# Kernel tuning notes

Hardware: AMD Instinct MI355X
Metric: run time of the kernel (lower is better)

## Reference

```python
import jax, jax.numpy as jnp
import numpy as np

NUM_HEADS = 8
NUM_LEVELS = 4
NUM_POINTS = 16
NUM_BEV = 2
EMBED = 256
BS = 64
NQ = NUM_LEVELS * NUM_POINTS  # 64


def _bilinear_sample(img, grid):
    """F.grid_sample(mode='bilinear', padding_mode='zeros', align_corners=False).
    img: (N, C, H, W); grid: (N, Hg, Wg, 2) in [-1, 1] (x, y). Returns (N, C, Hg, Wg)."""
    N, C, H, W = img.shape
    gx = (grid[..., 0] + 1.0) * (W * 0.5) - 0.5  # (N, Hg, Wg)
    gy = (grid[..., 1] + 1.0) * (H * 0.5) - 0.5
    x0 = jnp.floor(gx)
    y0 = jnp.floor(gy)
    flat = img.reshape(N, C, H * W)

    def gather(xi, yi):
        valid = (xi >= 0) & (xi <= W - 1) & (yi >= 0) & (yi <= H - 1)
        xc = jnp.clip(xi, 0, W - 1).astype(jnp.int32)
        yc = jnp.clip(yi, 0, H - 1).astype(jnp.int32)
        idx = (yc * W + xc).reshape(N, 1, -1)
        g = jnp.take_along_axis(flat, idx, axis=2).reshape(N, C, xi.shape[1], xi.shape[2])
        return g * valid[:, None, :, :].astype(img.dtype)

    wx1 = (gx - x0)[:, None]  # (N,1,Hg,Wg)
    wy1 = (gy - y0)[:, None]
    v00 = gather(x0, y0)
    v01 = gather(x0 + 1.0, y0)
    v10 = gather(x0, y0 + 1.0)
    v11 = gather(x0 + 1.0, y0 + 1.0)
    top = v00 * (1.0 - wx1) + v01 * wx1
    bot = v10 * (1.0 - wx1) + v11 * wx1
    return top * (1.0 - wy1) + bot * wy1


def _forward(query, key_hist, value_hist, reference_points, W_off, b_off, spatial_shapes):
    bs, nq, d = query.shape
    Hn, L, P, BEV = NUM_HEADS, NUM_LEVELS, NUM_POINTS, NUM_BEV
    dh = d // Hn
    Pb = P * BEV
    ss = np.asarray(spatial_shapes)  # (L, 2) static (h, w)

    queries = jnp.concatenate([query, query], axis=1)           # (bs, 2*nq, d)
    keies = jnp.concatenate([query, key_hist], axis=1)
    values = jnp.concatenate([query, value_hist], axis=1)
    qb = queries.shape[1]

    # sampling offsets projection (the only used learned linear in the original forward)
    off = (queries @ W_off + b_off).reshape(bs, qb, Hn, Pb, L, 2)

    # NOTE: original re-assigns q/k/v from the RAW concatenated tensors (to_Q/to_K/to_V discarded)
    qh = queries.reshape(bs, qb, Hn, dh)
    kh = keies.reshape(bs, qb, Hn, dh)
    vh = values.reshape(bs, qb, Hn, dh)

    attn = jax.nn.softmax(jnp.einsum('bqhd,bkhd->bqhk', qh, kh), axis=-1)
    attn = attn.reshape(bs, qb, Hn, L, Pb)

    rp = jnp.concatenate([reference_points, reference_points], axis=1)  # (bs, qb, L, 2)
    norm = jnp.stack([jnp.asarray(ss[:, 1], jnp.float32),
                      jnp.asarray(ss[:, 0], jnp.float32)], axis=-1)      # (L, 2) = (w, h)
    loc = rp[:, :, None, None, :, :] + off / norm                        # (bs,qb,H,Pb,L,2)
    # FAITHFUL: original uses .view here (pure reshape, not a transpose)
    loc = loc.reshape(bs, qb, Hn, L, Pb, 2)
    grids = 2.0 * loc - 1.0

    sampled = []
    start = 0
    for l in range(L):
        h_, w_ = int(ss[l, 0]), int(ss[l, 1])
        vl = vh[:, start:start + h_ * w_]                                # (bs, hw, H, dh)
        start += h_ * w_
        img = vl.transpose(0, 2, 3, 1).reshape(bs * Hn, dh, h_, w_)      # (bs*H, dh, h, w)
        grid_l = grids[:, :, :, l].transpose(0, 2, 1, 3, 4).reshape(bs * Hn, qb, Pb, 2)
        sampled.append(_bilinear_sample(img, grid_l))                    # (bs*H, dh, qb, Pb)

    samp = jnp.stack(sampled, axis=-2).reshape(bs * Hn, dh, qb, L * Pb)
    aw = attn.transpose(0, 2, 1, 3, 4).reshape(bs * Hn, 1, qb, L * Pb)
    out = (samp * aw).sum(-1)                                            # (bs*H, dh, qb)
    # FAITHFUL: original reshapes q_bev dim as (nq, BEV) and means over BEV
    out = out.reshape(bs, Hn * dh, nq, BEV).mean(-1).transpose(0, 2, 1)  # (bs, nq, d)
    return out + query  # dropout is identity at eval


def setup_inputs() -> dict:
    key = jax.random.key(0)
    ks = jax.random.split(key, 6)
    query = jax.random.normal(ks[0], (BS, NQ, EMBED), jnp.float32)
    key_hist = jax.random.normal(ks[1], (BS, NQ, EMBED), jnp.float32)
    value_hist = jax.random.normal(ks[2], (BS, NQ, EMBED), jnp.float32)
    reference_points = jax.random.uniform(ks[3], (BS, NQ, NUM_LEVELS, 2), jnp.float32)
    spatial_shapes = jnp.array([[4, 8]] * NUM_LEVELS, dtype=jnp.int32)  # sum(h*w)=128=L*P*BEV
    off_dim = NUM_HEADS * NUM_BEV * NUM_POINTS * NUM_LEVELS * 2
    W_off = jax.random.normal(ks[4], (EMBED, off_dim), jnp.float32) * 0.02
    b_off = jnp.zeros((off_dim,), jnp.float32)
    return {"query": query, "key_hist": key_hist, "value_hist": value_hist,
            "reference_points": reference_points, "spatial_shapes": spatial_shapes,
            "W_off": W_off, "b_off": b_off}


def reference(query, key_hist, value_hist, reference_points, spatial_shapes, W_off, b_off):
    return _forward(query, key_hist, value_hist, reference_points, W_off, b_off, spatial_shapes)
```

## Files before the change

### kernel.cpp

```cpp
#include <hip/hip_runtime.h>


typedef short  s16x8 __attribute__((ext_vector_type(8)));
typedef short  s16x4 __attribute__((ext_vector_type(4)));
typedef float  f32x4 __attribute__((ext_vector_type(4)));

__device__ __forceinline__ unsigned short f2bf(float f) {
    union { float f; unsigned u; } v; v.f = f;
    unsigned r = v.u + 0x7FFFu + ((v.u >> 16) & 1u);
    return (unsigned short)(r >> 16);
}
__device__ __forceinline__ float bf2f(unsigned short u) {
    return __uint_as_float(((unsigned)u) << 16);
}

__global__ __launch_bounds__(256) void prep(
    const float* __restrict__ W, const float* __restrict__ query,
    const float* __restrict__ key_hist,
    short* __restrict__ Wtb, short* __restrict__ Qb, short* __restrict__ Khb)
{
    __shared__ float s[32][33];
    const int bx = blockIdx.x, t = threadIdx.x;
    if (bx < 512) {
        const int n0 = (bx & 63) * 32, k0 = (bx >> 6) * 32;
        const int c = t & 31, r0 = t >> 5;
        #pragma unroll
        for (int p = 0; p < 4; ++p) {
            const int r = r0 + p * 8;
            s[r][c] = W[(size_t)(k0 + r) * 2048 + n0 + c];
        }
        __syncthreads();
        #pragma unroll
        for (int p = 0; p < 4; ++p) {
            const int r = r0 + p * 8;
            Wtb[(size_t)(n0 + r) * 256 + k0 + c] = (short)f2bf(s[c][r]);
        }
    } else {
        const int j = bx - 512;
        const bool isK = j >= 1024;
        const float* src = isK ? key_hist : query;
        short* dst = isK ? Khb : Qb;
        const int i4 = ((j & 1023) * 256 + t) * 4;
        const float4 v = *(const float4*)(src + i4);
        s16x4 o;
        o.x = (short)f2bf(v.x); o.y = (short)f2bf(v.y);
        o.z = (short)f2bf(v.z); o.w = (short)f2bf(v.w);
        *(s16x4*)(dst + i4) = o;
    }
}

__global__ __launch_bounds__(256, 2) void mega2(
    const float* __restrict__ query, const float* __restrict__ value_hist,
    const float* __restrict__ refp,
    const short* __restrict__ Qb, const short* __restrict__ Khb,
    const short* __restrict__ Wtb, const float* __restrict__ bias,
    float* __restrict__ out)
{
    const int h = blockIdx.x, b = blockIdx.y;
    const int t = threadIdx.x, lane = t & 63, wave = t >> 6;
    const int quad = lane >> 4, col = lane & 15;
    const int wq = wave * 16;

    __shared__ __align__(16) short VTl[32 * 136];
    __shared__ __align__(16) short attLb[64 * 136];
    __shared__ __align__(16) float rpsL[512];
    __shared__ __align__(16) float AmU[9216];
    short* Bsl = (short*)AmU;
    float* Am  = AmU;
    short* Amb = (short*)AmU;

    {
        const int p = t >> 1, hf = (t & 1) * 16;
        const float* src = ((p < 64) ? query : value_hist) +
                           (size_t)(b * 64 + (p & 63)) * 256 + h * 32 + hf;
        #pragma unroll
        for (int u = 0; u < 4; ++u) {
            const float4 v = *(const float4*)(src + 4 * u);
            VTl[(hf + 4 * u + 0) * 136 + p] = (short)f2bf(v.x);
            VTl[(hf + 4 * u + 1) * 136 + p] = (short)f2bf(v.y);
            VTl[(hf + 4 * u + 2) * 136 + p] = (short)f2bf(v.z);
            VTl[(hf + 4 * u + 3) * 136 + p] = (short)f2bf(v.w);
        }
    }
    rpsL[t]       = refp[(size_t)b * 512 + t];
    rpsL[t + 256] = refp[(size_t)b * 512 + t + 256];

    {
        const s16x8 aq = *(const s16x8*)(Qb +
            ((size_t)b * 64 + wq + col) * 256 + h * 32 + quad * 8);
        f32x4 lacc[8];
        #pragma unroll
        for (int t8 = 0; t8 < 8; ++t8) {
            const short* src = (t8 < 4)
                ? (Qb  + ((size_t)b * 64 + 16 * t8 + col) * 256)
                : (Khb + ((size_t)b * 64 + 16 * (t8 - 4) + col) * 256);
            const s16x8 bk = *(const s16x8*)(src + h * 32 + quad * 8);
            const f32x4 z = {0.f, 0.f, 0.f, 0.f};
            lacc[t8] = __builtin_amdgcn_mfma_f32_16x16x32_bf16(aq, bk, z, 0, 0, 0);
        }
        #pragma unroll
        for (int r = 0; r < 4; ++r) {
            float m = lacc[0][r];
            #pragma unroll
            for (int t8 = 1; t8 < 8; ++t8) m = fmaxf(m, lacc[t8][r]);
            #pragma unroll
            for (int s = 1; s < 16; s <<= 1) m = fmaxf(m, __shfl_xor(m, s, 64));
            float e[8], ssum = 0.f;
            #pragma unroll
            for (int t8 = 0; t8 < 8; ++t8) {
                e[t8] = __expf(lacc[t8][r] - m); ssum += e[t8];
            }
            #pragma unroll
            for (int s = 1; s < 16; s <<= 1) ssum += __shfl_xor(ssum, s, 64);
            const float inv = 1.0f / ssum;
            const int q = wq + 4 * quad + r;
            #pragma unroll
            for (int t8 = 0; t8 < 8; ++t8)
                attLb[q * 136 + 16 * t8 + col] = (short)f2bf(e[t8] * inv);
        }
    }

    f32x4 acc[4][4] = {};
    for (int kq = 0; kq < 4; ++kq) {
        s16x8 afp[4][2];
        #pragma unroll
        for (int mi = 0; mi < 4; ++mi)
            #pragma unroll
            for (int ks = 0; ks < 2; ++ks)
                afp[mi][ks] = *(const s16x8*)(Qb +
                    ((size_t)b * 64 + 16 * mi + col) * 256
                    + kq * 64 + ks * 32 + quad * 8);
        #pragma unroll
        for (int u = 0; u < 8; ++u) {
            const int g = t + 256 * u;
            const int w = g >> 9, rowu = (g >> 3) & 63, koff = (g & 7) * 8;
            *(s16x8*)&Bsl[(w * 64 + rowu) * 72 + koff] =
                *(const s16x8*)(Wtb + (size_t)(h * 256 + w * 64 + rowu) * 256
                                + kq * 64 + koff);
        }
        __syncthreads();
        #pragma unroll
        for (int ks = 0; ks < 2; ++ks) {
            s16x8 bf[4];
            #pragma unroll
            for (int nj = 0; nj < 4; ++nj)
                bf[nj] = *(const s16x8*)&Bsl[(wave * 64 + 16 * nj + col) * 72
                                             + ks * 32 + quad * 8];
            #pragma unroll
            for (int mi = 0; mi < 4; ++mi)
                #pragma unroll
                for (int nj = 0; nj < 4; ++nj)
                    acc[mi][nj] = __builtin_amdgcn_mfma_f32_16x16x32_bf16(
                        afp[mi][ks], bf[nj], acc[mi][nj], 0, 0, 0);
        }
        __syncthreads();
    }

    {
        #pragma unroll
        for (int u = 0; u < 33; ++u) AmU[t + 256 * u] = 0.f;
    }
    __syncthreads();
    {
        const int i   = col >> 1;
        const int par = col & 1;
        const int base = 32 * wave;
        #pragma unroll
        for (int nj = 0; nj < 4; ++nj) {
            const float bj = bias[h * 256 + wave * 64 + 16 * nj + col];
            const int f = 32 * wave + 8 * nj + i;
            #pragma unroll
            for (int mi = 0; mi < 4; ++mi) {
                float v[4], p[4];
                #pragma unroll
                for (int r = 0; r < 4; ++r) v[r] = acc[mi][nj][r] + bj;
                #pragma unroll
                for (int r = 0; r < 4; ++r) p[r] = __shfl_xor(v[r], 1, 64);
                #pragma unroll
                for (int rs = 0; rs < 2; ++rs) {
                    const int r = par * 2 + rs;
                    const float ox = par ? p[r] : v[r];
                    const float oy = par ? v[r] : p[r];
                    const int q = 16 * mi + 4 * quad + r;
                    const float2 rp = *(const float2*)&rpsL[q * 8 + (i & 3) * 2];
                    const float a = bf2f((unsigned short)attLb[q * 136 + f]);
                    const float gx = 8.f * (rp.x + ox * 0.125f) - 0.5f;
                    const float gy = 4.f * (rp.y + oy * 0.25f) - 0.5f;
                    const float x0f = floorf(gx), y0f = floorf(gy);
                    const float wx = gx - x0f, wy = gy - y0f;
                    const int x0 = (int)x0f, y0 = (int)y0f;
                    float* rowW = &Am[q * 132 + base];
                    const bool xv0 = (x0 >= 0) && (x0 < 8);
                    const bool xv1 = (x0 >= -1) && (x0 < 7);
                    const bool yv0 = (y0 >= 0) && (y0 < 4);
                    const bool yv1 = (y0 >= -1) && (y0 < 3);
                    if (xv0 && yv0) unsafeAtomicAdd(&rowW[y0 * 8 + x0],           a * (1.f - wx) * (1.f - wy));
                    if (xv1 && yv0) unsafeAtomicAdd(&rowW[y0 * 8 + x0 + 1],       a * wx * (1.f - wy));
                    if (xv0 && yv1) unsafeAtomicAdd(&rowW[(y0 + 1) * 8 + x0],     a * (1.f - wx) * wy);
                    if (xv1 && yv1) unsafeAtomicAdd(&rowW[(y0 + 1) * 8 + x0 + 1], a * wx * wy);
                }
            }
        }
    }
    __syncthreads();

    {
        const int cq = t >> 2, cc = (t & 3) * 32;
        float vreg[32];
        #pragma unroll
        for (int u = 0; u < 8; ++u) {
            const float4 v = *(const float4*)&Am[cq * 132 + cc + 4 * u];
            vreg[4 * u + 0] = v.x; vreg[4 * u + 1] = v.y;
            vreg[4 * u + 2] = v.z; vreg[4 * u + 3] = v.w;
        }
        __syncthreads();
        #pragma unroll
        for (int u = 0; u < 4; ++u) {
            s16x8 o;
            #pragma unroll
            for (int j = 0; j < 8; ++j) o[j] = (short)f2bf(vreg[u * 8 + j]);
            *(s16x8*)&Amb[cq * 136 + cc + u * 8] = o;
        }
    }
    __syncthreads();
    {
        f32x4 oacc[2] = {};
        #pragma unroll
        for (int ks = 0; ks < 4; ++ks) {
            const s16x8 af = *(const s16x8*)&Amb[(wq + col) * 136 + ks * 32 + quad * 8];
            #pragma unroll
            for (int n2 = 0; n2 < 2; ++n2) {
                const s16x8 bv = *(const s16x8*)&VTl[(n2 * 16 + col) * 136
                                                     + ks * 32 + quad * 8];
                oacc[n2] = __builtin_amdgcn_mfma_f32_16x16x32_bf16(af, bv, oacc[n2], 0, 0, 0);
            }
        }
        #pragma unroll
        for (int n2 = 0; n2 < 2; ++n2) {
            const int d = h * 32 + n2 * 16 + col;
            #pragma unroll
            for (int pr = 0; pr < 2; ++pr) {
                const float avg = 0.5f * (oacc[n2][2 * pr] + oacc[n2][2 * pr + 1]);
                const int pj = wave * 8 + quad * 2 + pr;
                const size_t re = ((size_t)b * 64 + pj) * 256 + d;
                const size_t ro = ((size_t)b * 64 + pj + 32) * 256 + d;
                out[re] = query[re] + avg;
                out[ro] = query[ro] + avg;
            }
        }
    }
}

extern "C" void kernel_launch(void* const* d_in, const int* in_sizes, int n_in,
                              void* d_out, int out_size, void* d_ws, size_t ws_size,
                              hipStream_t stream) {
    (void)in_sizes; (void)n_in; (void)out_size; (void)ws_size;
    const float* query      = (const float*)d_in[0];
    const float* key_hist   = (const float*)d_in[1];
    const float* value_hist = (const float*)d_in[2];
    const float* refp       = (const float*)d_in[3];
    const float* W_off      = (const float*)d_in[5];
    const float* b_off      = (const float*)d_in[6];

    char* ws = (char*)d_ws;
    short* Wtb = (short*)(ws);
    short* Qb  = (short*)(ws + (1u << 20));
    short* Khb = (short*)(ws + (3u << 20));
    float* out = (float*)d_out;

    prep<<<2560, 256, 0, stream>>>(W_off, query, key_hist, Wtb, Qb, Khb);
    mega2<<<dim3(8, 64), 256, 0, stream>>>(query, value_hist, refp,
                                           Qb, Khb, Wtb, b_off, out);
}
```

Baseline: 162.0 us.

## Make each wave own its query rows end-to-end, dropping LDS staging and block barriers

The offset projection GEMM is repartitioned so each wave computes all 256 output columns for its own 16 query rows, reading W fragments straight from global memory instead of staging them through LDS with block-wide barriers. Softmax probabilities stay in registers and are exchanged with lane shuffles rather than written to a shared attention buffer. The per-wave Am strip is private, so most __syncthreads are replaced by sched barriers. The smaller LDS footprint allows launch bounds of 3 blocks per CU. The cost is higher register pressure (16 accumulators plus 32 softmax values) and redundant global W reads across waves.

```diff
diff --git a/kernel.cpp b/kernel.cpp
--- a/kernel.cpp
+++ b/kernel.cpp
@@ -49,7 +49,7 @@
     }
 }
 
-__global__ __launch_bounds__(256, 2) void mega2(
+__global__ __launch_bounds__(256, 3) void mega3(
     const float* __restrict__ query, const float* __restrict__ value_hist,
     const float* __restrict__ refp,
     const short* __restrict__ Qb, const short* __restrict__ Khb,
@@ -62,12 +62,8 @@
     const int wq = wave * 16;
 
     __shared__ __align__(16) short VTl[32 * 136];
-    __shared__ __align__(16) short attLb[64 * 136];
     __shared__ __align__(16) float rpsL[512];
-    __shared__ __align__(16) float AmU[9216];
-    short* Bsl = (short*)AmU;
-    float* Am  = AmU;
-    short* Amb = (short*)AmU;
+    __shared__ __align__(16) float Am[64 * 132];
 
     {
         const int p = t >> 1, hf = (t & 1) * 16;
@@ -84,7 +80,42 @@
     }
     rpsL[t]       = refp[(size_t)b * 512 + t];
     rpsL[t + 256] = refp[(size_t)b * 512 + t + 256];
-
+    {
+        float* strip = &Am[wq * 132];
+        #pragma unroll
+        for (int u = 0; u < 33; ++u) strip[lane + 64 * u] = 0.f;
+    }
+
+    f32x4 acc[16];
+    #pragma unroll
+    for (int nj = 0; nj < 16; ++nj) acc[nj] = f32x4{0.f, 0.f, 0.f, 0.f};
+    {
+        const short* qrow = Qb + ((size_t)b * 64 + wq + col) * 256 + quad * 8;
+        const short* wrow = Wtb + ((size_t)(h * 256 + col)) * 256 + quad * 8;
+        for (int kq = 0; kq < 4; ++kq) {
+            const s16x8 a0 = *(const s16x8*)(qrow + kq * 64);
+            const s16x8 a1 = *(const s16x8*)(qrow + kq * 64 + 32);
+            #pragma unroll
+            for (int njc = 0; njc < 4; ++njc) {
+                s16x8 bf0[4], bf1[4];
+                #pragma unroll
+                for (int j = 0; j < 4; ++j) {
+                    const short* wp = wrow + (size_t)(njc * 4 + j) * 4096 + kq * 64;
+                    bf0[j] = *(const s16x8*)(wp);
+                    bf1[j] = *(const s16x8*)(wp + 32);
+                }
+                #pragma unroll
+                for (int j = 0; j < 4; ++j) {
+                    acc[njc * 4 + j] = __builtin_amdgcn_mfma_f32_16x16x32_bf16(
+                        a0, bf0[j], acc[njc * 4 + j], 0, 0, 0);
+                    acc[njc * 4 + j] = __builtin_amdgcn_mfma_f32_16x16x32_bf16(
+                        a1, bf1[j], acc[njc * 4 + j], 0, 0, 0);
+                }
+            }
+        }
+    }
+
+    float pro[8][4];
     {
         const s16x8 aq = *(const s16x8*)(Qb +
             ((size_t)b * 64 + wq + col) * 256 + h * 32 + quad * 8);
@@ -113,121 +144,85 @@
             #pragma unroll
             for (int s = 1; s < 16; s <<= 1) ssum += __shfl_xor(ssum, s, 64);
             const float inv = 1.0f / ssum;
-            const int q = wq + 4 * quad + r;
-            #pragma unroll
-            for (int t8 = 0; t8 < 8; ++t8)
-                attLb[q * 136 + 16 * t8 + col] = (short)f2bf(e[t8] * inv);
-        }
-    }
-
-    f32x4 acc[4][4] = {};
-    for (int kq = 0; kq < 4; ++kq) {
-        s16x8 afp[4][2];
-        #pragma unroll
-        for (int mi = 0; mi < 4; ++mi)
-            #pragma unroll
-            for (int ks = 0; ks < 2; ++ks)
-                afp[mi][ks] = *(const s16x8*)(Qb +
-                    ((size_t)b * 64 + 16 * mi + col) * 256
-                    + kq * 64 + ks * 32 + quad * 8);
-        #pragma unroll
-        for (int u = 0; u < 8; ++u) {
-            const int g = t + 256 * u;
-            const int w = g >> 9, rowu = (g >> 3) & 63, koff = (g & 7) * 8;
-            *(s16x8*)&Bsl[(w * 64 + rowu) * 72 + koff] =
-                *(const s16x8*)(Wtb + (size_t)(h * 256 + w * 64 + rowu) * 256
-                                + kq * 64 + koff);
-        }
-        __syncthreads();
-        #pragma unroll
-        for (int ks = 0; ks < 2; ++ks) {
-            s16x8 bf[4];
-            #pragma unroll
-            for (int nj = 0; nj < 4; ++nj)
-                bf[nj] = *(const s16x8*)&Bsl[(wave * 64 + 16 * nj + col) * 72
-                                             + ks * 32 + quad * 8];
-            #pragma unroll
-            for (int mi = 0; mi < 4; ++mi)
-                #pragma unroll
-                for (int nj = 0; nj < 4; ++nj)
-                    acc[mi][nj] = __builtin_amdgcn_mfma_f32_16x16x32_bf16(
-                        afp[mi][ks], bf[nj], acc[mi][nj], 0, 0, 0);
-        }
-        __syncthreads();
-    }
-
-    {
-        #pragma unroll
-        for (int u = 0; u < 33; ++u) AmU[t + 256 * u] = 0.f;
-    }
+            #pragma unroll
+            for (int t8 = 0; t8 < 8; ++t8) pro[t8][r] = e[t8] * inv;
+        }
+    }
+
+    float bjv[16];
+    #pragma unroll
+    for (int nj = 0; nj < 16; ++nj) bjv[nj] = bias[h * 256 + 16 * nj + col];
+
     __syncthreads();
+
     {
         const int i   = col >> 1;
         const int par = col & 1;
-        const int base = 32 * wave;
-        #pragma unroll
-        for (int nj = 0; nj < 4; ++nj) {
-            const float bj = bias[h * 256 + wave * 64 + 16 * nj + col];
-            const int f = 32 * wave + 8 * nj + i;
-            #pragma unroll
-            for (int mi = 0; mi < 4; ++mi) {
-                float v[4], p[4];
-                #pragma unroll
-                for (int r = 0; r < 4; ++r) v[r] = acc[mi][nj][r] + bj;
-                #pragma unroll
-                for (int r = 0; r < 4; ++r) p[r] = __shfl_xor(v[r], 1, 64);
-                #pragma unroll
-                for (int rs = 0; rs < 2; ++rs) {
-                    const int r = par * 2 + rs;
-                    const float ox = par ? p[r] : v[r];
-                    const float oy = par ? v[r] : p[r];
-                    const int q = 16 * mi + 4 * quad + r;
-                    const float2 rp = *(const float2*)&rpsL[q * 8 + (i & 3) * 2];
-                    const float a = bf2f((unsigned short)attLb[q * 136 + f]);
-                    const float gx = 8.f * (rp.x + ox * 0.125f) - 0.5f;
-                    const float gy = 4.f * (rp.y + oy * 0.25f) - 0.5f;
-                    const float x0f = floorf(gx), y0f = floorf(gy);
-                    const float wx = gx - x0f, wy = gy - y0f;
-                    const int x0 = (int)x0f, y0 = (int)y0f;
-                    float* rowW = &Am[q * 132 + base];
-                    const bool xv0 = (x0 >= 0) && (x0 < 8);
-                    const bool xv1 = (x0 >= -1) && (x0 < 7);
-                    const bool yv0 = (y0 >= 0) && (y0 < 4);
-                    const bool yv1 = (y0 >= -1) && (y0 < 3);
-                    if (xv0 && yv0) unsafeAtomicAdd(&rowW[y0 * 8 + x0],           a * (1.f - wx) * (1.f - wy));
-                    if (xv1 && yv0) unsafeAtomicAdd(&rowW[y0 * 8 + x0 + 1],       a * wx * (1.f - wy));
-                    if (xv0 && yv1) unsafeAtomicAdd(&rowW[(y0 + 1) * 8 + x0],     a * (1.f - wx) * wy);
-                    if (xv1 && yv1) unsafeAtomicAdd(&rowW[(y0 + 1) * 8 + x0 + 1], a * wx * wy);
-                }
-            }
-        }
-    }
-    __syncthreads();
-
-    {
-        const int cq = t >> 2, cc = (t & 3) * 32;
+        #pragma unroll
+        for (int nj = 0; nj < 16; ++nj) {
+            const int base = (nj >> 2) * 32;
+            const int srcl = quad * 16 + 8 * (nj & 1) + i;
+            float v[4], p[4];
+            #pragma unroll
+            for (int r = 0; r < 4; ++r) v[r] = acc[nj][r] + bjv[nj];
+            #pragma unroll
+            for (int r = 0; r < 4; ++r) p[r] = __shfl_xor(v[r], 1, 64);
+            #pragma unroll
+            for (int rs = 0; rs < 2; ++rs) {
+                const float a0s = __shfl(pro[nj >> 1][rs],     srcl, 64);
+                const float a1s = __shfl(pro[nj >> 1][2 + rs], srcl, 64);
+                const float a  = par ? a1s : a0s;
+                const float ox = par ? p[2 + rs] : v[rs];
+                const float oy = par ? v[2 + rs] : p[rs];
+                const int ql = 4 * quad + 2 * par + rs;
+                const float2 rp = *(const float2*)&rpsL[(wq + ql) * 8 + (i & 3) * 2];
+                const float gx = 8.f * (rp.x + ox * 0.125f) - 0.5f;
+                const float gy = 4.f * (rp.y + oy * 0.25f) - 0.5f;
+                const float x0f = floorf(gx), y0f = floorf(gy);
+                const float wx = gx - x0f, wy = gy - y0f;
+                const int x0 = (int)x0f, y0 = (int)y0f;
+                float* rowW = &Am[(wq + ql) * 132 + base];
+                const bool xv0 = (x0 >= 0) && (x0 < 8);
+                const bool xv1 = (x0 >= -1) && (x0 < 7);
+                const bool yv0 = (y0 >= 0) && (y0 < 4);
+                const bool yv1 = (y0 >= -1) && (y0 < 3);
+                if (xv0 && yv0) unsafeAtomicAdd(&rowW[y0 * 8 + x0],           a * (1.f - wx) * (1.f - wy));
+                if (xv1 && yv0) unsafeAtomicAdd(&rowW[y0 * 8 + x0 + 1],       a * wx * (1.f - wy));
+                if (xv0 && yv1) unsafeAtomicAdd(&rowW[(y0 + 1) * 8 + x0],     a * (1.f - wx) * wy);
+                if (xv1 && yv1) unsafeAtomicAdd(&rowW[(y0 + 1) * 8 + x0 + 1], a * wx * wy);
+            }
+        }
+    }
+    __builtin_amdgcn_sched_barrier(0);
+
+    {
+        float* strip = &Am[wq * 132];
+        const int row = lane >> 2, cc = (lane & 3) * 32;
         float vreg[32];
         #pragma unroll
         for (int u = 0; u < 8; ++u) {
-            const float4 v = *(const float4*)&Am[cq * 132 + cc + 4 * u];
-            vreg[4 * u + 0] = v.x; vreg[4 * u + 1] = v.y;
-            vreg[4 * u + 2] = v.z; vreg[4 * u + 3] = v.w;
-        }
-        __syncthreads();
+            const f32x4 vv = *(const f32x4*)&strip[row * 132 + cc + 4 * u];
+            vreg[4 * u + 0] = vv[0]; vreg[4 * u + 1] = vv[1];
+            vreg[4 * u + 2] = vv[2]; vreg[4 * u + 3] = vv[3];
+        }
+        __builtin_amdgcn_sched_barrier(0);
+        short* sb = (short*)strip;
         #pragma unroll
         for (int u = 0; u < 4; ++u) {
             s16x8 o;
             #pragma unroll
             for (int j = 0; j < 8; ++j) o[j] = (short)f2bf(vreg[u * 8 + j]);
-            *(s16x8*)&Amb[cq * 136 + cc + u * 8] = o;
-        }
-    }
-    __syncthreads();
-    {
+            *(s16x8*)&sb[row * 136 + cc + u * 8] = o;
+        }
+    }
+    __builtin_amdgcn_sched_barrier(0);
+
+    {
+        const short* sb = (const short*)&Am[wq * 132];
         f32x4 oacc[2] = {};
         #pragma unroll
         for (int ks = 0; ks < 4; ++ks) {
-            const s16x8 af = *(const s16x8*)&Amb[(wq + col) * 136 + ks * 32 + quad * 8];
+            const s16x8 af = *(const s16x8*)&sb[col * 136 + ks * 32 + quad * 8];
             #pragma unroll
             for (int n2 = 0; n2 < 2; ++n2) {
                 const s16x8 bv = *(const s16x8*)&VTl[(n2 * 16 + col) * 136
@@ -269,6 +264,6 @@
     float* out = (float*)d_out;
 
     prep<<<2560, 256, 0, stream>>>(W_off, query, key_hist, Wtb, Qb, Khb);
-    mega2<<<dim3(8, 64), 256, 0, stream>>>(query, value_hist, refp,
+    mega3<<<dim3(8, 64), 256, 0, stream>>>(query, value_hist, refp,
                                            Qb, Khb, Wtb, b_off, out);
 }
```

After: 183.1 us. +13.0%, slower.

## Load GEMM B fragments directly from global, drop LDS staging and aliasing

Applied to the files above, without the earlier changes.

The offset-projection GEMM now reads W fragments straight from global memory into registers instead of staging them through shared memory, so the per-k-step barriers go away. The GEMM is moved ahead of the softmax, the loop is fully unrolled, and bias loads are hoisted out of the loop. Am and Amb get separate shared buffers rather than one aliased union, which removes a barrier in the conversion step. In exchange the kernel uses more LDS and more registers, which may lower occupancy, and W is read from global with less coalescing.

```diff
diff --git a/kernel.cpp b/kernel.cpp
--- a/kernel.cpp
+++ b/kernel.cpp
@@ -49,7 +49,7 @@
     }
 }
 
-__global__ __launch_bounds__(256, 2) void mega2(
+__global__ __launch_bounds__(256, 2) void mega4(
     const float* __restrict__ query, const float* __restrict__ value_hist,
     const float* __restrict__ refp,
     const short* __restrict__ Qb, const short* __restrict__ Khb,
@@ -64,10 +64,8 @@
     __shared__ __align__(16) short VTl[32 * 136];
     __shared__ __align__(16) short attLb[64 * 136];
     __shared__ __align__(16) float rpsL[512];
-    __shared__ __align__(16) float AmU[9216];
-    short* Bsl = (short*)AmU;
-    float* Am  = AmU;
-    short* Amb = (short*)AmU;
+    __shared__ __align__(16) float Am[64 * 132];
+    __shared__ __align__(16) short Amb[64 * 136];
 
     {
         const int p = t >> 1, hf = (t & 1) * 16;
@@ -84,6 +82,36 @@
     }
     rpsL[t]       = refp[(size_t)b * 512 + t];
     rpsL[t + 256] = refp[(size_t)b * 512 + t + 256];
+    #pragma unroll
+    for (int u = 0; u < 33; ++u) Am[t + 256 * u] = 0.f;
+
+    f32x4 acc[4][4] = {};
+    #pragma unroll
+    for (int kq = 0; kq < 4; ++kq) {
+        s16x8 afp[4][2], bfp[4][2];
+        #pragma unroll
+        for (int mi = 0; mi < 4; ++mi)
+            #pragma unroll
+            for (int ks = 0; ks < 2; ++ks)
+                afp[mi][ks] = *(const s16x8*)(Qb +
+                    ((size_t)b * 64 + 16 * mi + col) * 256
+                    + kq * 64 + ks * 32 + quad * 8);
+        #pragma unroll
+        for (int nj = 0; nj < 4; ++nj)
+            #pragma unroll
+            for (int ks = 0; ks < 2; ++ks)
+                bfp[nj][ks] = *(const s16x8*)(Wtb +
+                    ((size_t)(h * 256 + wave * 64 + 16 * nj + col)) * 256
+                    + kq * 64 + ks * 32 + quad * 8);
+        #pragma unroll
+        for (int ks = 0; ks < 2; ++ks)
+            #pragma unroll
+            for (int mi = 0; mi < 4; ++mi)
+                #pragma unroll
+                for (int nj = 0; nj < 4; ++nj)
+                    acc[mi][nj] = __builtin_amdgcn_mfma_f32_16x16x32_bf16(
+                        afp[mi][ks], bfp[nj][ks], acc[mi][nj], 0, 0, 0);
+    }
 
     {
         const s16x8 aq = *(const s16x8*)(Qb +
@@ -120,60 +148,25 @@
         }
     }
 
-    f32x4 acc[4][4] = {};
-    for (int kq = 0; kq < 4; ++kq) {
-        s16x8 afp[4][2];
-        #pragma unroll
-        for (int mi = 0; mi < 4; ++mi)
-            #pragma unroll
-            for (int ks = 0; ks < 2; ++ks)
-                afp[mi][ks] = *(const s16x8*)(Qb +
-                    ((size_t)b * 64 + 16 * mi + col) * 256
-                    + kq * 64 + ks * 32 + quad * 8);
-        #pragma unroll
-        for (int u = 0; u < 8; ++u) {
-            const int g = t + 256 * u;
-            const int w = g >> 9, rowu = (g >> 3) & 63, koff = (g & 7) * 8;
-            *(s16x8*)&Bsl[(w * 64 + rowu) * 72 + koff] =
-                *(const s16x8*)(Wtb + (size_t)(h * 256 + w * 64 + rowu) * 256
-                                + kq * 64 + koff);
-        }
-        __syncthreads();
-        #pragma unroll
-        for (int ks = 0; ks < 2; ++ks) {
-            s16x8 bf[4];
-            #pragma unroll
-            for (int nj = 0; nj < 4; ++nj)
-                bf[nj] = *(const s16x8*)&Bsl[(wave * 64 + 16 * nj + col) * 72
-                                             + ks * 32 + quad * 8];
-            #pragma unroll
-            for (int mi = 0; mi < 4; ++mi)
-                #pragma unroll
-                for (int nj = 0; nj < 4; ++nj)
-                    acc[mi][nj] = __builtin_amdgcn_mfma_f32_16x16x32_bf16(
-                        afp[mi][ks], bf[nj], acc[mi][nj], 0, 0, 0);
-        }
-        __syncthreads();
-    }
-
-    {
-        #pragma unroll
-        for (int u = 0; u < 33; ++u) AmU[t + 256 * u] = 0.f;
-    }
+    float bjv[4];
+    #pragma unroll
+    for (int nj = 0; nj < 4; ++nj)
+        bjv[nj] = bias[h * 256 + wave * 64 + 16 * nj + col];
+
     __syncthreads();
+
     {
         const int i   = col >> 1;
         const int par = col & 1;
         const int base = 32 * wave;
         #pragma unroll
         for (int nj = 0; nj < 4; ++nj) {
-            const float bj = bias[h * 256 + wave * 64 + 16 * nj + col];
             const int f = 32 * wave + 8 * nj + i;
             #pragma unroll
             for (int mi = 0; mi < 4; ++mi) {
                 float v[4], p[4];
                 #pragma unroll
-                for (int r = 0; r < 4; ++r) v[r] = acc[mi][nj][r] + bj;
+                for (int r = 0; r < 4; ++r) v[r] = acc[mi][nj][r] + bjv[nj];
                 #pragma unroll
                 for (int r = 0; r < 4; ++r) p[r] = __shfl_xor(v[r], 1, 64);
                 #pragma unroll
@@ -206,23 +199,20 @@
 
     {
         const int cq = t >> 2, cc = (t & 3) * 32;
-        float vreg[32];
-        #pragma unroll
-        for (int u = 0; u < 8; ++u) {
-            const float4 v = *(const float4*)&Am[cq * 132 + cc + 4 * u];
-            vreg[4 * u + 0] = v.x; vreg[4 * u + 1] = v.y;
-            vreg[4 * u + 2] = v.z; vreg[4 * u + 3] = v.w;
-        }
-        __syncthreads();
         #pragma unroll
         for (int u = 0; u < 4; ++u) {
+            const f32x4 v0 = *(const f32x4*)&Am[cq * 132 + cc + 8 * u];
+            const f32x4 v1 = *(const f32x4*)&Am[cq * 132 + cc + 8 * u + 4];
             s16x8 o;
-            #pragma unroll
-            for (int j = 0; j < 8; ++j) o[j] = (short)f2bf(vreg[u * 8 + j]);
+            o[0] = (short)f2bf(v0[0]); o[1] = (short)f2bf(v0[1]);
+            o[2] = (short)f2bf(v0[2]); o[3] = (short)f2bf(v0[3]);
+            o[4] = (short)f2bf(v1[0]); o[5] = (short)f2bf(v1[1]);
+            o[6] = (short)f2bf(v1[2]); o[7] = (short)f2bf(v1[3]);
             *(s16x8*)&Amb[cq * 136 + cc + u * 8] = o;
         }
     }
     __syncthreads();
+
     {
         f32x4 oacc[2] = {};
         #pragma unroll
@@ -269,6 +259,6 @@
     float* out = (float*)d_out;
 
     prep<<<2560, 256, 0, stream>>>(W_off, query, key_hist, Wtb, Qb, Khb);
-    mega2<<<dim3(8, 64), 256, 0, stream>>>(query, value_hist, refp,
+    mega4<<<dim3(8, 64), 256, 0, stream>>>(query, value_hist, refp,
                                            Qb, Khb, Wtb, b_off, out);
 }
```

Result: slower. 165.7 us (+2.3%).
